# Optimization experiments

Hardware: AMD Instinct MI355X
Metric: run time of the kernel (lower is better)

## Reference

```python
import jax, jax.numpy as jnp
import numpy as np

DIM = 512
HID = 1536          # int(2*(4*512)/3) rounded up to multiple of 256
N_EXPERTS = 8
TOP_K = 2
SHARED_HID = HID * 2  # n_shared_experts scales hidden dim of the single shared MLP
B, S = 4, 2048


def _swiglu(x, w1, w3, w2):
    return (jax.nn.silu(x @ w1.T) * (x @ w3.T)) @ w2.T


def setup_inputs() -> dict:
    key = jax.random.key(0)
    ks = jax.random.split(key, 8)
    sc_d = 1.0 / np.sqrt(DIM)
    sc_h = 1.0 / np.sqrt(HID)
    sc_sh = 1.0 / np.sqrt(SHARED_HID)
    return {
        "x": jax.random.normal(ks[0], (B, S, DIM), jnp.float32),
        "gate_w": jax.random.normal(ks[1], (N_EXPERTS, DIM), jnp.float32) * sc_d,
        "w1": jax.random.normal(ks[2], (N_EXPERTS, HID, DIM), jnp.float32) * sc_d,
        "w3": jax.random.normal(ks[3], (N_EXPERTS, HID, DIM), jnp.float32) * sc_d,
        "w2": jax.random.normal(ks[4], (N_EXPERTS, DIM, HID), jnp.float32) * sc_h,
        "sw1": jax.random.normal(ks[5], (SHARED_HID, DIM), jnp.float32) * sc_d,
        "sw3": jax.random.normal(ks[6], (SHARED_HID, DIM), jnp.float32) * sc_d,
        "sw2": jax.random.normal(ks[7], (DIM, SHARED_HID), jnp.float32) * sc_sh,
    }


def reference(x, gate_w, w1, w3, w2, sw1, sw3, sw2):
    b, s, d = x.shape
    t = b * s
    xf = x.reshape(t, d)

    # --- gate (greedy top-k over softmax scores, fp32) ---
    logits = xf.astype(jnp.float32) @ gate_w.astype(jnp.float32).T  # [T, E]
    scores = jax.nn.softmax(logits, axis=-1)
    topk_w, topk_i = jax.lax.top_k(scores, TOP_K)                    # [T, K]

    # per-token combine weight for each expert: sum of topk weights routed to it
    e = gate_w.shape[0]
    comb = jnp.zeros((t, e), jnp.float32).at[jnp.arange(t)[:, None], topk_i].add(topk_w)

    # --- routed experts: weighted sum of SwiGLU outputs ---
    y = jnp.zeros((t, d), x.dtype)
    for i in range(e):  # fixed small number of structurally distinct experts
        ye = _swiglu(xf, w1[i], w3[i], w2[i]).astype(x.dtype)
        y = y + comb[:, i:i + 1].astype(x.dtype) * ye
    y = y.reshape(b, s, d)

    # --- shared expert added to all tokens ---
    shared = _swiglu(xf, sw1, sw3, sw2).reshape(b, s, d).astype(x.dtype)
    return y + shared
```

## Files before the change

### kernel.cpp

```cpp
#include <hip/hip_runtime.h>

#define T_TOK 8192
#define DIMSZ 512
#define HIDSZ 1536
#define SHIDSZ 3072
#define NE 8

typedef __attribute__((ext_vector_type(4))) float f32x4;
typedef __attribute__((ext_vector_type(8))) short s16x8;

__device__ __forceinline__ unsigned short f2bf(float f) {
  unsigned int u = __float_as_uint(f);
  u += 0x7fff + ((u >> 16) & 1);
  return (unsigned short)(u >> 16);
}

__device__ __forceinline__ void async16(void* lds, const void* g) {
  __builtin_amdgcn_global_load_lds((const __attribute__((address_space(1))) void*)g,
                                   (__attribute__((address_space(3))) void*)lds,
                                   16, 0, 0);
}

__global__ void cvt_bf16(const float* __restrict__ s, unsigned short* __restrict__ d, int n4) {
  int i = blockIdx.x * blockDim.x + threadIdx.x;
  if (i < n4) {
    float4 v = ((const float4*)s)[i];
    ushort4 o;
    o.x = f2bf(v.x); o.y = f2bf(v.y); o.z = f2bf(v.z); o.w = f2bf(v.w);
    ((ushort4*)d)[i] = o;
  }
}

#define GATE_BLOCKS 256
#define GATE_TPB (T_TOK / GATE_BLOCKS)
#define GATE_TPW (GATE_TPB / 4)

__global__ __launch_bounds__(256) void gate_kernel(
    const float* __restrict__ x, const float* __restrict__ gw,
    float* __restrict__ tw, int* __restrict__ ti, int* __restrict__ cnt) {
  __shared__ int lcnt[NE];
  const int tid = threadIdx.x;
  if (tid < NE) lcnt[tid] = 0;
  __syncthreads();
  const int w = tid >> 6, l = tid & 63;

  float gv[NE][8];
  const float* gbase = gw + l * 8;
#pragma unroll
  for (int e = 0; e < NE; ++e)
#pragma unroll
    for (int j = 0; j < 8; ++j) gv[e][j] = gbase[e * DIMSZ + j];

  const int tok0 = blockIdx.x * GATE_TPB + w * GATE_TPW;
  for (int it = 0; it < GATE_TPW; ++it) {
    const int t = tok0 + it;
    const float* xr = x + (size_t)t * DIMSZ + l * 8;
    float xv[8];
#pragma unroll
    for (int j = 0; j < 8; ++j) xv[j] = xr[j];
    float p[NE];
#pragma unroll
    for (int e = 0; e < NE; ++e) {
      float s = 0.f;
#pragma unroll
      for (int j = 0; j < 8; ++j) s = fmaf(xv[j], gv[e][j], s);
      p[e] = s;
    }
#pragma unroll
    for (int e = 0; e < NE; ++e) {
      float v = p[e];
#pragma unroll
      for (int off = 32; off > 0; off >>= 1) v += __shfl_xor(v, off);
      p[e] = v;
    }
    float m = p[0];
#pragma unroll
    for (int e = 1; e < NE; ++e) m = fmaxf(m, p[e]);
    float ex[NE], s = 0.f;
#pragma unroll
    for (int e = 0; e < NE; ++e) { ex[e] = __expf(p[e] - m); s += ex[e]; }
    float inv = 1.f / s;
    int e0 = 0; float v0 = p[0];
#pragma unroll
    for (int e = 1; e < NE; ++e) if (p[e] > v0) { v0 = p[e]; e0 = e; }
    int e1 = -1; float v1 = -3.4e38f;
#pragma unroll
    for (int e = 0; e < NE; ++e) if (e != e0 && p[e] > v1) { v1 = p[e]; e1 = e; }
    if (l == 0) {
      ti[2 * t] = e0;     tw[2 * t] = ex[e0] * inv;
      ti[2 * t + 1] = e1; tw[2 * t + 1] = ex[e1] * inv;
      atomicAdd(&lcnt[e0], 1);
      atomicAdd(&lcnt[e1], 1);
    }
  }
  __syncthreads();
  if (tid < NE) atomicAdd(&cnt[tid], lcnt[tid]);
}

__global__ void scan_kernel(const int* __restrict__ cnt, int* __restrict__ base,
                            int* __restrict__ cursor) {
  if (threadIdx.x == 0 && blockIdx.x == 0) {
    int r = 0;
    for (int e = 0; e < NE; ++e) { base[e] = r; cursor[e] = r; r += cnt[e]; }
  }
}

__global__ __launch_bounds__(256) void scatter_kernel(
    const int* __restrict__ ti, int* __restrict__ cursor,
    int* __restrict__ tok, int* __restrict__ dst) {
  __shared__ int lcnt[NE], gbase[NE];
  const int tid = threadIdx.x;
  if (tid < NE) lcnt[tid] = 0;
  __syncthreads();
  const int t = blockIdx.x * 256 + tid;
  const int e0 = ti[2 * t], e1 = ti[2 * t + 1];
  const int p0 = atomicAdd(&lcnt[e0], 1);
  const int p1 = atomicAdd(&lcnt[e1], 1);
  __syncthreads();
  if (tid < NE) gbase[tid] = atomicAdd(&cursor[tid], lcnt[tid]);
  __syncthreads();
  const int i0 = gbase[e0] + p0, i1 = gbase[e1] + p1;
  tok[i0] = t; dst[i0] = 2 * t;
  tok[i1] = t; dst[i1] = 2 * t + 1;
}

__global__ void gather_kernel(const unsigned short* __restrict__ xb,
                              const int* __restrict__ tok,
                              unsigned short* __restrict__ xg) {
  int i = blockIdx.x * blockDim.x + threadIdx.x;
  int entry = i >> 6, l = i & 63;
  int t = tok[entry];
  ((uint4*)xg)[entry * 64 + l] = ((const uint4*)xb)[t * 64 + l];
}

template <bool ROUTED>
__global__ __launch_bounds__(256, 2) void gemm1_kernel(
    const unsigned short* __restrict__ A0, const unsigned short* __restrict__ W1,
    const unsigned short* __restrict__ W3, unsigned short* __restrict__ G,
    const int* __restrict__ cnt, const int* __restrict__ base,
    int K, int N, int mtPerE) {
  int e, mt, cntE, rowbase;
  if constexpr (ROUTED) {
    e = blockIdx.x / mtPerE; mt = blockIdx.x % mtPerE;
    cntE = cnt[e];
    if (mt * 128 >= cntE) return;
    rowbase = base[e];
  } else {
    e = 0; mt = blockIdx.x; cntE = T_TOK; rowbase = 0;
  }
  const int m0 = mt * 128;
  const int n0 = blockIdx.y * 128;
  const unsigned short* A = A0 + (size_t)rowbase * K;
  const unsigned short* B1 = W1 + (size_t)e * N * K + (size_t)n0 * K;
  const unsigned short* B3 = W3 + (size_t)e * N * K + (size_t)n0 * K;

  __shared__ __align__(16) unsigned short As[128 * 32];
  __shared__ __align__(16) unsigned short B1s[128 * 32];
  __shared__ __align__(16) unsigned short B3s[128 * 32];

  const int tid = threadIdx.x;
  const int w = tid >> 6, lane = tid & 63;
  const int wr = w >> 1, wc = w & 1;
  const int lhi = lane >> 4, llo = lane & 15;

  const int idx0 = w * 128 + lane;
  const int idx1 = idx0 + 64;
  const int ra0 = idx0 >> 2, ca0 = (idx0 & 3) * 8;
  const int ra1 = idx1 >> 2, ca1 = (idx1 & 3) * 8;
  const int ar0 = ROUTED ? min(m0 + ra0, cntE - 1) : (m0 + ra0);
  const int ar1 = ROUTED ? min(m0 + ra1, cntE - 1) : (m0 + ra1);

  const unsigned short* gA0 = A + (size_t)ar0 * K + ca0;
  const unsigned short* gA1 = A + (size_t)ar1 * K + ca1;
  const unsigned short* gB1a = B1 + (size_t)ra0 * K + ca0;
  const unsigned short* gB1b = B1 + (size_t)ra1 * K + ca1;
  const unsigned short* gB3a = B3 + (size_t)ra0 * K + ca0;
  const unsigned short* gB3b = B3 + (size_t)ra1 * K + ca1;
  unsigned short* lA0 = &As[(w * 128) * 8];
  unsigned short* lA1 = &As[(w * 128 + 64) * 8];
  unsigned short* lB1a = &B1s[(w * 128) * 8];
  unsigned short* lB1b = &B1s[(w * 128 + 64) * 8];
  unsigned short* lB3a = &B3s[(w * 128) * 8];
  unsigned short* lB3b = &B3s[(w * 128 + 64) * 8];

  f32x4 acc1[4][4], acc3[4][4];
#pragma unroll
  for (int i = 0; i < 4; ++i)
#pragma unroll
    for (int j = 0; j < 4; ++j) {
      acc1[i][j] = f32x4{0.f, 0.f, 0.f, 0.f};
      acc3[i][j] = f32x4{0.f, 0.f, 0.f, 0.f};
    }

  for (int k0 = 0; k0 < K; k0 += 32) {
    async16(lA0, gA0 + k0);
    async16(lA1, gA1 + k0);
    async16(lB1a, gB1a + k0);
    async16(lB1b, gB1b + k0);
    async16(lB3a, gB3a + k0);
    async16(lB3b, gB3b + k0);
    __syncthreads();
    s16x8 a[4], b1[4], b3[4];
#pragma unroll
    for (int i = 0; i < 4; ++i)
      a[i] = *(const s16x8*)&As[(wr * 64 + i * 16 + llo) * 32 + lhi * 8];
#pragma unroll
    for (int j = 0; j < 4; ++j) {
      b1[j] = *(const s16x8*)&B1s[(wc * 64 + j * 16 + llo) * 32 + lhi * 8];
      b3[j] = *(const s16x8*)&B3s[(wc * 64 + j * 16 + llo) * 32 + lhi * 8];
    }
#pragma unroll
    for (int i = 0; i < 4; ++i)
#pragma unroll
      for (int j = 0; j < 4; ++j) {
        acc1[i][j] = __builtin_amdgcn_mfma_f32_16x16x32_bf16(a[i], b1[j], acc1[i][j], 0, 0, 0);
        acc3[i][j] = __builtin_amdgcn_mfma_f32_16x16x32_bf16(a[i], b3[j], acc3[i][j], 0, 0, 0);
      }
    __syncthreads();
  }

  unsigned short* Grow = G + (size_t)rowbase * N;
#pragma unroll
  for (int i = 0; i < 4; ++i)
#pragma unroll
    for (int j = 0; j < 4; ++j)
#pragma unroll
      for (int q = 0; q < 4; ++q) {
        int r = wr * 64 + i * 16 + lhi * 4 + q;
        if (!ROUTED || (m0 + r) < cntE) {
          float h1 = acc1[i][j][q], h3 = acc3[i][j][q];
          float val = (h1 / (1.f + __expf(-h1))) * h3;
          Grow[(size_t)(m0 + r) * N + n0 + wc * 64 + j * 16 + llo] = f2bf(val);
        }
      }
}

template <bool ROUTED>
__global__ __launch_bounds__(256, 2) void gemm2_kernel(
    const unsigned short* __restrict__ A0, const unsigned short* __restrict__ W2,
    float* __restrict__ Out, const int* __restrict__ cnt, const int* __restrict__ base,
    const int* __restrict__ dst, int K, int mtPerE) {
  int e, mt, cntE, rowbase;
  if constexpr (ROUTED) {
    e = blockIdx.x / mtPerE; mt = blockIdx.x % mtPerE;
    cntE = cnt[e];
    if (mt * 128 >= cntE) return;
    rowbase = base[e];
  } else {
    e = 0; mt = blockIdx.x; cntE = T_TOK; rowbase = 0;
  }
  const int m0 = mt * 128;
  const int n0 = blockIdx.y * 128;
  const unsigned short* A = A0 + (size_t)rowbase * K;
  const unsigned short* B = W2 + (size_t)e * DIMSZ * K + (size_t)n0 * K;

  __shared__ __align__(16) unsigned short As[128 * 32];
  __shared__ __align__(16) unsigned short Bs[128 * 32];

  const int tid = threadIdx.x;
  const int w = tid >> 6, lane = tid & 63;
  const int wr = w >> 1, wc = w & 1;
  const int lhi = lane >> 4, llo = lane & 15;

  const int idx0 = w * 128 + lane;
  const int idx1 = idx0 + 64;
  const int ra0 = idx0 >> 2, ca0 = (idx0 & 3) * 8;
  const int ra1 = idx1 >> 2, ca1 = (idx1 & 3) * 8;
  const int ar0 = ROUTED ? min(m0 + ra0, cntE - 1) : (m0 + ra0);
  const int ar1 = ROUTED ? min(m0 + ra1, cntE - 1) : (m0 + ra1);

  const unsigned short* gA0 = A + (size_t)ar0 * K + ca0;
  const unsigned short* gA1 = A + (size_t)ar1 * K + ca1;
  const unsigned short* gBa = B + (size_t)ra0 * K + ca0;
  const unsigned short* gBb = B + (size_t)ra1 * K + ca1;
  unsigned short* lA0 = &As[(w * 128) * 8];
  unsigned short* lA1 = &As[(w * 128 + 64) * 8];
  unsigned short* lBa = &Bs[(w * 128) * 8];
  unsigned short* lBb = &Bs[(w * 128 + 64) * 8];

  f32x4 acc[4][4];
#pragma unroll
  for (int i = 0; i < 4; ++i)
#pragma unroll
    for (int j = 0; j < 4; ++j) acc[i][j] = f32x4{0.f, 0.f, 0.f, 0.f};

  for (int k0 = 0; k0 < K; k0 += 32) {
    async16(lA0, gA0 + k0);
    async16(lA1, gA1 + k0);
    async16(lBa, gBa + k0);
    async16(lBb, gBb + k0);
    __syncthreads();
    s16x8 a[4], b[4];
#pragma unroll
    for (int i = 0; i < 4; ++i)
      a[i] = *(const s16x8*)&As[(wr * 64 + i * 16 + llo) * 32 + lhi * 8];
#pragma unroll
    for (int j = 0; j < 4; ++j)
      b[j] = *(const s16x8*)&Bs[(wc * 64 + j * 16 + llo) * 32 + lhi * 8];
#pragma unroll
    for (int i = 0; i < 4; ++i)
#pragma unroll
      for (int j = 0; j < 4; ++j)
        acc[i][j] = __builtin_amdgcn_mfma_f32_16x16x32_bf16(a[i], b[j], acc[i][j], 0, 0, 0);
    __syncthreads();
  }

#pragma unroll
  for (int i = 0; i < 4; ++i)
#pragma unroll
    for (int j = 0; j < 4; ++j)
#pragma unroll
      for (int q = 0; q < 4; ++q) {
        int r = wr * 64 + i * 16 + lhi * 4 + q;
        if (!ROUTED || (m0 + r) < cntE) {
          int orow;
          if constexpr (ROUTED) orow = dst[rowbase + m0 + r];
          else                  orow = m0 + r;
          Out[(size_t)orow * DIMSZ + n0 + wc * 64 + j * 16 + llo] = acc[i][j][q];
        }
      }
}

__global__ void combine_kernel(const float* __restrict__ shbuf, const float* __restrict__ pair,
                               const float* __restrict__ tw, float* __restrict__ out) {
  int i = blockIdx.x * blockDim.x + threadIdx.x;
  int t = i >> 7, c = i & 127;
  float w0 = tw[2 * t], w1 = tw[2 * t + 1];
  float4 a = ((const float4*)shbuf)[i];
  float4 p0 = ((const float4*)pair)[(size_t)(2 * t) * 128 + c];
  float4 p1 = ((const float4*)pair)[(size_t)(2 * t + 1) * 128 + c];
  float4 o;
  o.x = a.x + w0 * p0.x + w1 * p1.x;
  o.y = a.y + w0 * p0.y + w1 * p1.y;
  o.z = a.z + w0 * p0.z + w1 * p1.z;
  o.w = a.w + w0 * p0.w + w1 * p1.w;
  ((float4*)out)[i] = o;
}

extern "C" void kernel_launch(void* const* d_in, const int* in_sizes, int n_in,
                              void* d_out, int out_size, void* d_ws, size_t ws_size,
                              hipStream_t stream) {
  const float* x   = (const float*)d_in[0];
  const float* gw  = (const float*)d_in[1];
  const float* w1  = (const float*)d_in[2];
  const float* w3  = (const float*)d_in[3];
  const float* w2  = (const float*)d_in[4];
  const float* sw1 = (const float*)d_in[5];
  const float* sw3 = (const float*)d_in[6];
  const float* sw2 = (const float*)d_in[7];
  float* out = (float*)d_out;

  char* p = (char*)d_ws;
  auto alloc = [&](size_t bytes) {
    char* r = p;
    p += (bytes + 255) & ~(size_t)255;
    return r;
  };
  unsigned short* xb   = (unsigned short*)alloc((size_t)T_TOK * DIMSZ * 2);
  unsigned short* xg   = (unsigned short*)alloc((size_t)2 * T_TOK * DIMSZ * 2);
  unsigned short* w1b  = (unsigned short*)alloc((size_t)NE * HIDSZ * DIMSZ * 2);
  unsigned short* w3b  = (unsigned short*)alloc((size_t)NE * HIDSZ * DIMSZ * 2);
  unsigned short* w2b  = (unsigned short*)alloc((size_t)NE * DIMSZ * HIDSZ * 2);
  unsigned short* sw1b = (unsigned short*)alloc((size_t)SHIDSZ * DIMSZ * 2);
  unsigned short* sw3b = (unsigned short*)alloc((size_t)SHIDSZ * DIMSZ * 2);
  unsigned short* sw2b = (unsigned short*)alloc((size_t)DIMSZ * SHIDSZ * 2);
  unsigned short* g    = (unsigned short*)alloc((size_t)T_TOK * SHIDSZ * 2);
  float* pairout = (float*)alloc((size_t)2 * T_TOK * DIMSZ * 4);
  float* shbuf   = (float*)alloc((size_t)T_TOK * DIMSZ * 4);
  float* tw = (float*)alloc((size_t)2 * T_TOK * 4);
  int* ti   = (int*)alloc((size_t)2 * T_TOK * 4);
  int* tok  = (int*)alloc((size_t)2 * T_TOK * 4);
  int* dst  = (int*)alloc((size_t)2 * T_TOK * 4);
  int* meta = (int*)alloc(256);
  int* cnt = meta, *cursor = meta + 8, *base = meta + 16;

  auto cvt = [&](const float* s, unsigned short* d, size_t n) {
    int n4 = (int)(n / 4);
    cvt_bf16<<<(n4 + 255) / 256, 256, 0, stream>>>(s, d, n4);
  };
  cvt(x, xb, (size_t)T_TOK * DIMSZ);
  cvt(w1, w1b, (size_t)NE * HIDSZ * DIMSZ);
  cvt(w3, w3b, (size_t)NE * HIDSZ * DIMSZ);
  cvt(w2, w2b, (size_t)NE * DIMSZ * HIDSZ);
  cvt(sw1, sw1b, (size_t)SHIDSZ * DIMSZ);
  cvt(sw3, sw3b, (size_t)SHIDSZ * DIMSZ);
  cvt(sw2, sw2b, (size_t)DIMSZ * SHIDSZ);

  hipMemsetAsync(meta, 0, 64, stream);
  gate_kernel<<<GATE_BLOCKS, 256, 0, stream>>>(x, gw, tw, ti, cnt);
  scan_kernel<<<1, 64, 0, stream>>>(cnt, base, cursor);
  scatter_kernel<<<T_TOK / 256, 256, 0, stream>>>(ti, cursor, tok, dst);
  gather_kernel<<<(2 * T_TOK * 64) / 256, 256, 0, stream>>>(xb, tok, xg);

  gemm1_kernel<false><<<dim3(T_TOK / 128, SHIDSZ / 128), 256, 0, stream>>>(
      xb, sw1b, sw3b, g, nullptr, nullptr, DIMSZ, SHIDSZ, T_TOK / 128);
  gemm2_kernel<false><<<dim3(T_TOK / 128, DIMSZ / 128), 256, 0, stream>>>(
      g, sw2b, shbuf, nullptr, nullptr, nullptr, SHIDSZ, T_TOK / 128);

  gemm1_kernel<true><<<dim3(NE * (T_TOK / 128), HIDSZ / 128), 256, 0, stream>>>(
      xg, w1b, w3b, g, cnt, base, DIMSZ, HIDSZ, T_TOK / 128);
  gemm2_kernel<true><<<dim3(NE * (T_TOK / 128), DIMSZ / 128), 256, 0, stream>>>(
      g, w2b, pairout, cnt, base, dst, HIDSZ, T_TOK / 128);

  combine_kernel<<<(T_TOK * 128) / 256, 256, 0, stream>>>(shbuf, pairout, tw, out);
}
```

Before: 526.2 us.

## Use K=64 tiles with XOR-swizzled LDS and narrower N tile in gate GEMM

Both GEMM kernels now load 64-wide K slices per iteration, which halves the number of barrier pairs. The LDS layout is XOR-swizzled on 16-byte chunks so fragment reads avoid bank conflicts. The gate/up GEMM narrows its N tile from 128 to 64, doubling its grid and cutting accumulator registers, and launch bounds rise to 3 blocks per CU for higher occupancy. The costs are reloading A twice as often in gemm1 and more LDS per block, which may limit how many blocks actually fit per CU.

```diff
diff --git a/kernel.cpp b/kernel.cpp
--- a/kernel.cpp
+++ b/kernel.cpp
@@ -133,8 +133,9 @@
   ((uint4*)xg)[entry * 64 + l] = ((const uint4*)xb)[t * 64 + l];
 }
 
+
 template <bool ROUTED>
-__global__ __launch_bounds__(256, 2) void gemm1_kernel(
+__global__ __launch_bounds__(256, 3) void gemm1_kernel(
     const unsigned short* __restrict__ A0, const unsigned short* __restrict__ W1,
     const unsigned short* __restrict__ W3, unsigned short* __restrict__ G,
     const int* __restrict__ cnt, const int* __restrict__ base,
@@ -149,94 +150,113 @@
     e = 0; mt = blockIdx.x; cntE = T_TOK; rowbase = 0;
   }
   const int m0 = mt * 128;
-  const int n0 = blockIdx.y * 128;
+  const int n0 = blockIdx.y * 64;
   const unsigned short* A = A0 + (size_t)rowbase * K;
   const unsigned short* B1 = W1 + (size_t)e * N * K + (size_t)n0 * K;
   const unsigned short* B3 = W3 + (size_t)e * N * K + (size_t)n0 * K;
 
-  __shared__ __align__(16) unsigned short As[128 * 32];
-  __shared__ __align__(16) unsigned short B1s[128 * 32];
-  __shared__ __align__(16) unsigned short B3s[128 * 32];
+  __shared__ __align__(16) unsigned short As[128 * 64];
+  __shared__ __align__(16) unsigned short B1s[64 * 64];
+  __shared__ __align__(16) unsigned short B3s[64 * 64];
 
   const int tid = threadIdx.x;
   const int w = tid >> 6, lane = tid & 63;
   const int wr = w >> 1, wc = w & 1;
   const int lhi = lane >> 4, llo = lane & 15;
 
-  const int idx0 = w * 128 + lane;
-  const int idx1 = idx0 + 64;
-  const int ra0 = idx0 >> 2, ca0 = (idx0 & 3) * 8;
-  const int ra1 = idx1 >> 2, ca1 = (idx1 & 3) * 8;
-  const int ar0 = ROUTED ? min(m0 + ra0, cntE - 1) : (m0 + ra0);
-  const int ar1 = ROUTED ? min(m0 + ra1, cntE - 1) : (m0 + ra1);
-
-  const unsigned short* gA0 = A + (size_t)ar0 * K + ca0;
-  const unsigned short* gA1 = A + (size_t)ar1 * K + ca1;
-  const unsigned short* gB1a = B1 + (size_t)ra0 * K + ca0;
-  const unsigned short* gB1b = B1 + (size_t)ra1 * K + ca1;
-  const unsigned short* gB3a = B3 + (size_t)ra0 * K + ca0;
-  const unsigned short* gB3b = B3 + (size_t)ra1 * K + ca1;
-  unsigned short* lA0 = &As[(w * 128) * 8];
-  unsigned short* lA1 = &As[(w * 128 + 64) * 8];
-  unsigned short* lB1a = &B1s[(w * 128) * 8];
-  unsigned short* lB1b = &B1s[(w * 128 + 64) * 8];
-  unsigned short* lB3a = &B3s[(w * 128) * 8];
-  unsigned short* lB3b = &B3s[(w * 128 + 64) * 8];
-
-  f32x4 acc1[4][4], acc3[4][4];
-#pragma unroll
-  for (int i = 0; i < 4; ++i)
-#pragma unroll
-    for (int j = 0; j < 4; ++j) {
-      acc1[i][j] = f32x4{0.f, 0.f, 0.f, 0.f};
-      acc3[i][j] = f32x4{0.f, 0.f, 0.f, 0.f};
-    }
-
-  for (int k0 = 0; k0 < K; k0 += 32) {
-    async16(lA0, gA0 + k0);
-    async16(lA1, gA1 + k0);
-    async16(lB1a, gB1a + k0);
-    async16(lB1b, gB1b + k0);
-    async16(lB3a, gB3a + k0);
-    async16(lB3b, gB3b + k0);
+  const unsigned short* aSrc[4];
+  unsigned short* aDst[4];
+#pragma unroll
+  for (int i = 0; i < 4; ++i) {
+    int L = i * 256 + tid, row = L >> 3, c = L & 7, sc = c ^ (row & 7);
+    int ar = ROUTED ? min(m0 + row, cntE - 1) : (m0 + row);
+    aSrc[i] = A + (size_t)ar * K + sc * 8;
+    aDst[i] = &As[(size_t)(i * 256 + (tid & ~63)) * 8];
+  }
+  const unsigned short *b1Src[2], *b3Src[2];
+  unsigned short *b1Dst[2], *b3Dst[2];
+#pragma unroll
+  for (int i = 0; i < 2; ++i) {
+    int L = i * 256 + tid, row = L >> 3, c = L & 7, sc = c ^ (row & 7);
+    b1Src[i] = B1 + (size_t)row * K + sc * 8;
+    b3Src[i] = B3 + (size_t)row * K + sc * 8;
+    b1Dst[i] = &B1s[(size_t)(i * 256 + (tid & ~63)) * 8];
+    b3Dst[i] = &B3s[(size_t)(i * 256 + (tid & ~63)) * 8];
+  }
+
+  int aOff[4][2], bOff[2][2];
+#pragma unroll
+  for (int m = 0; m < 4; ++m) {
+    int r = wr * 64 + m * 16 + llo;
+#pragma unroll
+    for (int s = 0; s < 2; ++s)
+      aOff[m][s] = r * 64 + (((lhi + 4 * s) ^ (r & 7)) * 8);
+  }
+#pragma unroll
+  for (int n = 0; n < 2; ++n) {
+    int r = wc * 32 + n * 16 + llo;
+#pragma unroll
+    for (int s = 0; s < 2; ++s)
+      bOff[n][s] = r * 64 + (((lhi + 4 * s) ^ (r & 7)) * 8);
+  }
+
+  f32x4 acc1[4][2], acc3[4][2];
+#pragma unroll
+  for (int m = 0; m < 4; ++m)
+#pragma unroll
+    for (int n = 0; n < 2; ++n) {
+      acc1[m][n] = f32x4{0.f, 0.f, 0.f, 0.f};
+      acc3[m][n] = f32x4{0.f, 0.f, 0.f, 0.f};
+    }
+
+  for (int k0 = 0; k0 < K; k0 += 64) {
+#pragma unroll
+    for (int i = 0; i < 4; ++i) async16(aDst[i], aSrc[i] + k0);
+#pragma unroll
+    for (int i = 0; i < 2; ++i) {
+      async16(b1Dst[i], b1Src[i] + k0);
+      async16(b3Dst[i], b3Src[i] + k0);
+    }
     __syncthreads();
-    s16x8 a[4], b1[4], b3[4];
-#pragma unroll
-    for (int i = 0; i < 4; ++i)
-      a[i] = *(const s16x8*)&As[(wr * 64 + i * 16 + llo) * 32 + lhi * 8];
-#pragma unroll
-    for (int j = 0; j < 4; ++j) {
-      b1[j] = *(const s16x8*)&B1s[(wc * 64 + j * 16 + llo) * 32 + lhi * 8];
-      b3[j] = *(const s16x8*)&B3s[(wc * 64 + j * 16 + llo) * 32 + lhi * 8];
-    }
-#pragma unroll
-    for (int i = 0; i < 4; ++i)
-#pragma unroll
-      for (int j = 0; j < 4; ++j) {
-        acc1[i][j] = __builtin_amdgcn_mfma_f32_16x16x32_bf16(a[i], b1[j], acc1[i][j], 0, 0, 0);
-        acc3[i][j] = __builtin_amdgcn_mfma_f32_16x16x32_bf16(a[i], b3[j], acc3[i][j], 0, 0, 0);
+#pragma unroll
+    for (int s = 0; s < 2; ++s) {
+      s16x8 a[4], b1f[2], b3f[2];
+#pragma unroll
+      for (int m = 0; m < 4; ++m) a[m] = *(const s16x8*)&As[aOff[m][s]];
+#pragma unroll
+      for (int n = 0; n < 2; ++n) {
+        b1f[n] = *(const s16x8*)&B1s[bOff[n][s]];
+        b3f[n] = *(const s16x8*)&B3s[bOff[n][s]];
       }
+#pragma unroll
+      for (int m = 0; m < 4; ++m)
+#pragma unroll
+        for (int n = 0; n < 2; ++n) {
+          acc1[m][n] = __builtin_amdgcn_mfma_f32_16x16x32_bf16(a[m], b1f[n], acc1[m][n], 0, 0, 0);
+          acc3[m][n] = __builtin_amdgcn_mfma_f32_16x16x32_bf16(a[m], b3f[n], acc3[m][n], 0, 0, 0);
+        }
+    }
     __syncthreads();
   }
 
   unsigned short* Grow = G + (size_t)rowbase * N;
 #pragma unroll
-  for (int i = 0; i < 4; ++i)
-#pragma unroll
-    for (int j = 0; j < 4; ++j)
+  for (int m = 0; m < 4; ++m)
+#pragma unroll
+    for (int n = 0; n < 2; ++n)
 #pragma unroll
       for (int q = 0; q < 4; ++q) {
-        int r = wr * 64 + i * 16 + lhi * 4 + q;
+        int r = wr * 64 + m * 16 + lhi * 4 + q;
         if (!ROUTED || (m0 + r) < cntE) {
-          float h1 = acc1[i][j][q], h3 = acc3[i][j][q];
+          float h1 = acc1[m][n][q], h3 = acc3[m][n][q];
           float val = (h1 / (1.f + __expf(-h1))) * h3;
-          Grow[(size_t)(m0 + r) * N + n0 + wc * 64 + j * 16 + llo] = f2bf(val);
+          Grow[(size_t)(m0 + r) * N + n0 + wc * 32 + n * 16 + llo] = f2bf(val);
         }
       }
 }
 
 template <bool ROUTED>
-__global__ __launch_bounds__(256, 2) void gemm2_kernel(
+__global__ __launch_bounds__(256, 3) void gemm2_kernel(
     const unsigned short* __restrict__ A0, const unsigned short* __restrict__ W2,
     float* __restrict__ Out, const int* __restrict__ cnt, const int* __restrict__ base,
     const int* __restrict__ dst, int K, int mtPerE) {
@@ -254,29 +274,37 @@
   const unsigned short* A = A0 + (size_t)rowbase * K;
   const unsigned short* B = W2 + (size_t)e * DIMSZ * K + (size_t)n0 * K;
 
-  __shared__ __align__(16) unsigned short As[128 * 32];
-  __shared__ __align__(16) unsigned short Bs[128 * 32];
+  __shared__ __align__(16) unsigned short As[128 * 64];
+  __shared__ __align__(16) unsigned short Bs[128 * 64];
 
   const int tid = threadIdx.x;
   const int w = tid >> 6, lane = tid & 63;
   const int wr = w >> 1, wc = w & 1;
   const int lhi = lane >> 4, llo = lane & 15;
 
-  const int idx0 = w * 128 + lane;
-  const int idx1 = idx0 + 64;
-  const int ra0 = idx0 >> 2, ca0 = (idx0 & 3) * 8;
-  const int ra1 = idx1 >> 2, ca1 = (idx1 & 3) * 8;
-  const int ar0 = ROUTED ? min(m0 + ra0, cntE - 1) : (m0 + ra0);
-  const int ar1 = ROUTED ? min(m0 + ra1, cntE - 1) : (m0 + ra1);
-
-  const unsigned short* gA0 = A + (size_t)ar0 * K + ca0;
-  const unsigned short* gA1 = A + (size_t)ar1 * K + ca1;
-  const unsigned short* gBa = B + (size_t)ra0 * K + ca0;
-  const unsigned short* gBb = B + (size_t)ra1 * K + ca1;
-  unsigned short* lA0 = &As[(w * 128) * 8];
-  unsigned short* lA1 = &As[(w * 128 + 64) * 8];
-  unsigned short* lBa = &Bs[(w * 128) * 8];
-  unsigned short* lBb = &Bs[(w * 128 + 64) * 8];
+  const unsigned short *aSrc[4], *bSrc[4];
+  unsigned short *aDst[4], *bDst[4];
+#pragma unroll
+  for (int i = 0; i < 4; ++i) {
+    int L = i * 256 + tid, row = L >> 3, c = L & 7, sc = c ^ (row & 7);
+    int ar = ROUTED ? min(m0 + row, cntE - 1) : (m0 + row);
+    aSrc[i] = A + (size_t)ar * K + sc * 8;
+    bSrc[i] = B + (size_t)row * K + sc * 8;
+    aDst[i] = &As[(size_t)(i * 256 + (tid & ~63)) * 8];
+    bDst[i] = &Bs[(size_t)(i * 256 + (tid & ~63)) * 8];
+  }
+
+  int aOff[4][2], bOff[4][2];
+#pragma unroll
+  for (int m = 0; m < 4; ++m) {
+    int ra = wr * 64 + m * 16 + llo;
+    int rb = wc * 64 + m * 16 + llo;
+#pragma unroll
+    for (int s = 0; s < 2; ++s) {
+      aOff[m][s] = ra * 64 + (((lhi + 4 * s) ^ (ra & 7)) * 8);
+      bOff[m][s] = rb * 64 + (((lhi + 4 * s) ^ (rb & 7)) * 8);
+    }
+  }
 
   f32x4 acc[4][4];
 #pragma unroll
@@ -284,24 +312,27 @@
 #pragma unroll
     for (int j = 0; j < 4; ++j) acc[i][j] = f32x4{0.f, 0.f, 0.f, 0.f};
 
-  for (int k0 = 0; k0 < K; k0 += 32) {
-    async16(lA0, gA0 + k0);
-    async16(lA1, gA1 + k0);
-    async16(lBa, gBa + k0);
-    async16(lBb, gBb + k0);
+  for (int k0 = 0; k0 < K; k0 += 64) {
+#pragma unroll
+    for (int i = 0; i < 4; ++i) {
+      async16(aDst[i], aSrc[i] + k0);
+      async16(bDst[i], bSrc[i] + k0);
+    }
     __syncthreads();
-    s16x8 a[4], b[4];
-#pragma unroll
-    for (int i = 0; i < 4; ++i)
-      a[i] = *(const s16x8*)&As[(wr * 64 + i * 16 + llo) * 32 + lhi * 8];
-#pragma unroll
-    for (int j = 0; j < 4; ++j)
-      b[j] = *(const s16x8*)&Bs[(wc * 64 + j * 16 + llo) * 32 + lhi * 8];
-#pragma unroll
-    for (int i = 0; i < 4; ++i)
-#pragma unroll
-      for (int j = 0; j < 4; ++j)
-        acc[i][j] = __builtin_amdgcn_mfma_f32_16x16x32_bf16(a[i], b[j], acc[i][j], 0, 0, 0);
+#pragma unroll
+    for (int s = 0; s < 2; ++s) {
+      s16x8 a[4], b[4];
+#pragma unroll
+      for (int m = 0; m < 4; ++m) {
+        a[m] = *(const s16x8*)&As[aOff[m][s]];
+        b[m] = *(const s16x8*)&Bs[bOff[m][s]];
+      }
+#pragma unroll
+      for (int i = 0; i < 4; ++i)
+#pragma unroll
+        for (int j = 0; j < 4; ++j)
+          acc[i][j] = __builtin_amdgcn_mfma_f32_16x16x32_bf16(a[i], b[j], acc[i][j], 0, 0, 0);
+    }
     __syncthreads();
   }
 
@@ -392,12 +423,12 @@
   scatter_kernel<<<T_TOK / 256, 256, 0, stream>>>(ti, cursor, tok, dst);
   gather_kernel<<<(2 * T_TOK * 64) / 256, 256, 0, stream>>>(xb, tok, xg);
 
-  gemm1_kernel<false><<<dim3(T_TOK / 128, SHIDSZ / 128), 256, 0, stream>>>(
+  gemm1_kernel<false><<<dim3(T_TOK / 128, SHIDSZ / 64), 256, 0, stream>>>(
       xb, sw1b, sw3b, g, nullptr, nullptr, DIMSZ, SHIDSZ, T_TOK / 128);
   gemm2_kernel<false><<<dim3(T_TOK / 128, DIMSZ / 128), 256, 0, stream>>>(
       g, sw2b, shbuf, nullptr, nullptr, nullptr, SHIDSZ, T_TOK / 128);
 
-  gemm1_kernel<true><<<dim3(NE * (T_TOK / 128), HIDSZ / 128), 256, 0, stream>>>(
+  gemm1_kernel<true><<<dim3(NE * (T_TOK / 128), HIDSZ / 64), 256, 0, stream>>>(
       xg, w1b, w3b, g, cnt, base, DIMSZ, HIDSZ, T_TOK / 128);
   gemm2_kernel<true><<<dim3(NE * (T_TOK / 128), DIMSZ / 128), 256, 0, stream>>>(
       g, w2b, pairout, cnt, base, dst, HIDSZ, T_TOK / 128);
```

New measurement: 448.7 us. -14.7%, faster.
